# Kernel optimization log

Measured on AMD Instinct MI355X. Metric: run time of the kernel, lower is better.

The kernel has to match this reference:

```python
import jax, jax.numpy as jnp
import numpy as np
import math

B, S, DIM = 1, 2048, 4096
N_HEADS, N_KV, HEAD_DIM = 32, 8, 128
WINDOW = 2048
ROPE_THETA = 10000.0


def setup_inputs() -> dict:
    key = jax.random.key(0)
    ks = jax.random.split(key, 6)
    w_std = 0.02
    x = jax.random.normal(ks[0], (B, S, DIM), dtype=jnp.float32)
    wq = jax.random.normal(ks[1], (DIM, N_HEADS * HEAD_DIM), dtype=jnp.float32) * w_std
    wk = jax.random.normal(ks[2], (DIM, N_KV * HEAD_DIM), dtype=jnp.float32) * w_std
    wv = jax.random.normal(ks[3], (DIM, N_KV * HEAD_DIM), dtype=jnp.float32) * w_std
    wo = jax.random.normal(ks[4], (N_HEADS * HEAD_DIM, DIM), dtype=jnp.float32) * w_std
    # rotary tables (real/imag of complex_rotary_matrix)
    pos = jnp.arange(S, dtype=jnp.float32)
    inv_freq = 1.0 / (ROPE_THETA ** (jnp.arange(0, HEAD_DIM, 2, dtype=jnp.float32) / HEAD_DIM))
    angles = pos[:, None] * inv_freq[None, :]  # [S, HEAD_DIM/2]
    cos, sin = jnp.cos(angles), jnp.sin(angles)
    positions = jnp.arange(S, dtype=jnp.int32)
    # sliding-window causal additive mask: allow j <= i and i - j < WINDOW
    i = jnp.arange(S)[:, None]
    j = jnp.arange(S)[None, :]
    allowed = (j <= i) & (i - j < WINDOW)
    mask = jnp.where(allowed, 0.0, -jnp.inf).astype(jnp.float32)
    cache_k = jnp.zeros((B, WINDOW, N_KV, HEAD_DIM), dtype=jnp.float32)
    cache_v = jnp.zeros((B, WINDOW, N_KV, HEAD_DIM), dtype=jnp.float32)
    return dict(x=x, wq=wq, wk=wk, wv=wv, wo=wo, cos=cos, sin=sin,
                positions=positions, mask=mask, cache_k=cache_k, cache_v=cache_v)


def _apply_rope(t, cos, sin):
    # t: [B, S, H, D]; interleaved complex pairs as in torch.view_as_complex
    tp = t.reshape(*t.shape[:-1], HEAD_DIM // 2, 2)
    te, to = tp[..., 0], tp[..., 1]
    c = cos[None, :, None, :]
    s = sin[None, :, None, :]
    re = te * c - to * s
    im = te * s + to * c
    return jnp.stack([re, im], axis=-1).reshape(t.shape)


def reference(x, wq, wk, wv, wo, cos, sin, positions, mask, cache_k, cache_v):
    repeats = N_HEADS // N_KV
    q = (x @ wq).reshape(B, S, N_HEADS, HEAD_DIM)
    k = (x @ wk).reshape(B, S, N_KV, HEAD_DIM)
    v = (x @ wv).reshape(B, S, N_KV, HEAD_DIM)
    q = _apply_rope(q, cos, sin)
    k = _apply_rope(k, cos, sin)
    # rolling KV-cache scatter update (prefill path: positions.shape[0] > 1)
    scatter_pos = positions[-WINDOW:] % WINDOW
    new_cache_k = cache_k.at[:, scatter_pos].set(k[:, -WINDOW:])
    new_cache_v = cache_v.at[:, scatter_pos].set(v[:, -WINDOW:])
    # GQA head repetition (repeat_kv_head)
    k = jnp.repeat(k, repeats, axis=2)  # [B, S, N_HEADS, D]
    v = jnp.repeat(v, repeats, axis=2)
    scores = jnp.einsum('bqhd,bkhd->bhqk', q, k) / math.sqrt(HEAD_DIM)
    scores = scores + mask[None, None, :, :]
    attn = jax.nn.softmax(scores.astype(jnp.float32), axis=-1).astype(q.dtype)
    out = jnp.einsum('bhqk,bkhd->bqhd', attn, v)
    out = out.reshape(B, S, N_HEADS * HEAD_DIM)
    return out @ wo, new_cache_k, new_cache_v
```

## Files before the change

### kernel.cpp

```cpp
#include <hip/hip_runtime.h>

typedef __bf16 bf16;
typedef __bf16 bf16x8 __attribute__((ext_vector_type(8)));
typedef __bf16 bf16x4 __attribute__((ext_vector_type(4)));
typedef float  f32x4  __attribute__((ext_vector_type(4)));

__device__ __forceinline__ f32x4 mfma16(bf16x8 a, bf16x8 b, f32x4 c) {
  return __builtin_amdgcn_mfma_f32_16x16x32_bf16(a, b, c, 0, 0, 0);
}

__device__ __forceinline__ void gload16(const bf16* g, bf16* l) {
  __builtin_amdgcn_global_load_lds(
      (const __attribute__((address_space(1))) void*)g,
      (__attribute__((address_space(3))) void*)l, 16, 0, 0);
}

__device__ __forceinline__ void tc64_body(const float* __restrict__ in,
                                          bf16* __restrict__ out,
                                          int ldin, int ldout, int bx, int by,
                                          bf16 (*t)[68]) {
  const int c0 = bx * 64, r0 = by * 64;
  const int g4 = threadIdx.x & 15;
  const int q  = threadIdx.x >> 4;
  #pragma unroll
  for (int i = 0; i < 4; ++i) {
    const int r = q + i * 16;
    const float4 v = *(const float4*)&in[(size_t)(r0 + r) * ldin + c0 + g4 * 4];
    bf16x4 b;
    b[0] = (bf16)v.x; b[1] = (bf16)v.y; b[2] = (bf16)v.z; b[3] = (bf16)v.w;
    *(bf16x4*)&t[r][g4 * 4] = b;
  }
  __syncthreads();
  #pragma unroll
  for (int i = 0; i < 4; ++i) {
    const int c = q + i * 16;
    bf16x4 b;
    b[0] = t[g4 * 4 + 0][c]; b[1] = t[g4 * 4 + 1][c];
    b[2] = t[g4 * 4 + 2][c]; b[3] = t[g4 * 4 + 3][c];
    *(bf16x4*)&out[(size_t)(c0 + c) * ldout + r0 + g4 * 4] = b;
  }
}

__global__ void prep1(const float* __restrict__ x, bf16* __restrict__ xb,
                      const float* __restrict__ wq, const float* __restrict__ wk,
                      const float* __restrict__ wv, bf16* __restrict__ wT) {
  __shared__ bf16 t[64][68];
  const int b = blockIdx.x;
  if (b < 8192) {
    const int i = b * 256 + threadIdx.x;
    const float4 v = ((const float4*)x)[i];
    bf16x4 o;
    o[0] = (bf16)v.x; o[1] = (bf16)v.y; o[2] = (bf16)v.z; o[3] = (bf16)v.w;
    *(bf16x4*)&xb[(size_t)i * 4] = o;
  } else if (b < 12288) {
    const int bb = b - 8192;
    tc64_body(wq, wT, 4096, 4096, bb & 63, bb >> 6, t);
  } else if (b < 13312) {
    const int bb = b - 12288;
    tc64_body(wk, wT + (size_t)16777216, 1024, 4096, bb & 15, bb >> 4, t);
  } else {
    const int bb = b - 13312;
    tc64_body(wv, wT + (size_t)20971520, 1024, 4096, bb & 15, bb >> 4, t);
  }
}

__global__ void prep2(bf16* __restrict__ qkv, bf16* __restrict__ kp,
                      float* __restrict__ ck, bf16* __restrict__ vp,
                      float* __restrict__ cv, const float* __restrict__ wo,
                      bf16* __restrict__ wT, const float* __restrict__ cs,
                      const float* __restrict__ sn) {
  __shared__ bf16 t[64][68];
  const int b = blockIdx.x;
  if (b < 16384) {
    const int idx = b * 256 + threadIdx.x;
    const int p  = idx & 63;
    const int sh = idx >> 6;
    const int h  = sh & 31;
    const int s  = sh >> 5;
    const float c  = cs[s * 64 + p];
    const float si = sn[s * 64 + p];
    const size_t ii = (size_t)s * 6144 + h * 128 + 2 * p;
    const float te = (float)qkv[ii], to = (float)qkv[ii + 1];
    qkv[ii]     = (bf16)(te * c - to * si);
    qkv[ii + 1] = (bf16)(te * si + to * c);
  } else if (b < 20480) {
    const int idx = (b - 16384) * 256 + threadIdx.x;
    const int p  = idx & 63;
    const int sh = idx >> 6;
    const int h  = sh & 7;
    const int s  = sh >> 3;
    const float c  = cs[s * 64 + p];
    const float si = sn[s * 64 + p];
    const size_t ii = (size_t)s * 6144 + 4096 + h * 128 + 2 * p;
    const float te = (float)qkv[ii], to = (float)qkv[ii + 1];
    const float re = te * c - to * si;
    const float im = te * si + to * c;
    const size_t io = ((size_t)(h * 4 + (p >> 4)) * 2048 + s) * 32 + ((2 * p) & 31);
    kp[io]     = (bf16)re;
    kp[io + 1] = (bf16)im;
    const size_t ic = (size_t)s * 1024 + h * 128 + 2 * p;
    ck[ic]     = re;
    ck[ic + 1] = im;
  } else if (b < 22528) {
    bf16 (*t32)[33] = (bf16(*)[33])&t[0][0];
    const int bb  = b - 20480;
    const int sb  = bb & 63;
    const int yy  = bb >> 6;
    const int kvh = yy >> 2;
    const int dt  = yy & 3;
    const int x = threadIdx.x & 31, y = threadIdx.x >> 5;
    #pragma unroll
    for (int i = 0; i < 32; i += 8) {
      const bf16 v = qkv[(size_t)(sb * 32 + y + i) * 6144 + 5120 +
                         kvh * 128 + dt * 32 + x];
      t32[y + i][x] = v;
      cv[(size_t)(sb * 32 + y + i) * 1024 + kvh * 128 + dt * 32 + x] = (float)v;
    }
    __syncthreads();
    #pragma unroll
    for (int i = 0; i < 32; i += 8)
      vp[((size_t)(kvh * 64 + sb) * 128 + dt * 32 + y + i) * 32 + x] = t32[x][y + i];
  } else {
    const int bb = b - 22528;
    tc64_body(wo, wT, 4096, 4096, bb & 63, bb >> 6, t);
  }
}

#define MMQ(MB, NB)                                                            \
  _Pragma("unroll")                                                            \
  for (int mi = 0; mi < 4; ++mi)                                               \
    _Pragma("unroll")                                                          \
    for (int ni = 0; ni < 2; ++ni)                                             \
      _Pragma("unroll")                                                        \
      for (int kk = 0; kk < 2; ++kk)                                           \
        acc[MB + mi][NB + ni] =                                                \
            mfma16(ar[mi][kk], br[NB + ni][kk], acc[MB + mi][NB + ni]);

#define MMQ1(MB)                                                               \
  _Pragma("unroll")                                                            \
  for (int mi = 0; mi < 4; ++mi)                                               \
    _Pragma("unroll")                                                          \
    for (int kk = 0; kk < 2; ++kk)                                             \
      acc[MB + mi][2] = mfma16(ar[mi][kk], br[2][kk], acc[MB + mi][2]);

#define PH_OPEN                                                                \
  __builtin_amdgcn_s_barrier();                                                \
  asm volatile("s_waitcnt lgkmcnt(0)" ::: "memory");                           \
  __builtin_amdgcn_s_setprio(1);

#define PH_CLOSE                                                               \
  __builtin_amdgcn_s_setprio(0);                                               \
  __builtin_amdgcn_s_barrier();

template <typename OutT, int NSPLIT>
__global__ __launch_bounds__(512, 2)
void gemm8(const bf16* __restrict__ A, const bf16* __restrict__ Bt,
           OutT* __restrict__ C0, OutT* __restrict__ C1,
           int M, int N, int K, int ldc) {
  __shared__ __attribute__((aligned(16))) bf16 lds[65536];
  char* ldsc = (char*)lds;
  constexpr int AO0 = 0, BO0 = 32768, AO1 = 65536, BO1 = 98304;

  const int t    = threadIdx.x;
  const int w    = t >> 6;
  const int lane = t & 63;
  const int l15  = lane & 15;
  const int lg   = lane >> 4;
  const int wm   = w >> 2;
  const int wn   = w & 3;
  const int hb   = wn >> 1;

  const int nbm = M >> 8;
  const int nb2 = nbm * NSPLIT;
  const int cpx = (nb2 * (N >> 8)) >> 3;
  const int lid = ((int)blockIdx.x & 7) * cpx + ((int)blockIdx.x >> 3);
  const int bn  = (lid / nb2) * 256;
  const int rem = lid % nb2;
  const int kh  = rem / nbm;
  const int bm  = (rem % nbm) * 256;
  const int Kloc = K / NSPLIT;
  const int koff = kh * Kloc;
  OutT* __restrict__ C = (NSPLIT == 2 && kh) ? C1 : C0;

  const int d0     = t * 16;
  const int dsw    = d0 ^ (((d0 >> 9) & 1) << 5);
  const int srow_s = (dsw >> 6) & 127;
  const int scol_e = (dsw & 63) >> 1;

  auto stg = [&](const bf16* P, int rowbase, int tile, int half, int region) {
    const bf16* s = P + (size_t)(rowbase + half * 128 + srow_s) * K +
                    koff + tile * 64 + scol_e;
    gload16(s,      (bf16*)(ldsc + region + half * 16384 + w * 1024));
    gload16(s + 32, (bf16*)(ldsc + region + half * 16384 + 8192 + w * 1024));
  };
  auto lda = [&](int AO, int m, int kk) -> bf16x8 {
    int byte = AO + wm * 16384 + kk * 8192 + (m * 16 + l15) * 64 + lg * 16;
    byte ^= ((byte >> 9) & 1) << 5;
    return *(const bf16x8*)(ldsc + byte);
  };
  auto ldb = [&](int BO, int n, int kk) -> bf16x8 {
    int byte = BO + hb * 16384 + kk * 8192 +
               ((wn & 1) * 64 + n * 16 + l15) * 64 + lg * 16;
    byte ^= ((byte >> 9) & 1) << 5;
    return *(const bf16x8*)(ldsc + byte);
  };

  f32x4 acc[8][4] = {};
  bf16x8 ar[4][2], br[4][2];

  const int NT = Kloc >> 6;
  const int NI = Kloc >> 7;

  stg(A,  bm, 0, 0, AO0);  stg(A,  bm, 0, 1, AO0);
  stg(Bt, bn, 0, 0, BO0);  stg(Bt, bn, 0, 1, BO0);
  stg(Bt, bn, 1, 0, BO1);  stg(Bt, bn, 1, 1, BO1);
  asm volatile("s_waitcnt vmcnt(4)" ::: "memory");
  __builtin_amdgcn_s_barrier();

  #pragma unroll 1
  for (int it = 0; it < NI; ++it) {
    const int t1 = 2 * it + 1;
    const int t2 = (2 * it + 2 < NT) ? 2 * it + 2 : NT - 1;
    const int t3 = (2 * it + 3 < NT) ? 2 * it + 3 : NT - 1;

    #pragma unroll
    for (int mi = 0; mi < 4; ++mi) {
      ar[mi][0] = lda(AO0, mi, 0); ar[mi][1] = lda(AO0, mi, 1);
    }
    #pragma unroll
    for (int ni = 0; ni < 2; ++ni) {
      br[ni][0] = ldb(BO0, ni, 0); br[ni][1] = ldb(BO0, ni, 1);
    }
    stg(A, bm, t1, 0, AO1);
    PH_OPEN; MMQ(0, 0); PH_CLOSE;
    #pragma unroll
    for (int ni = 2; ni < 4; ++ni) {
      br[ni][0] = ldb(BO0, ni, 0); br[ni][1] = ldb(BO0, ni, 1);
    }
    stg(A, bm, t1, 1, AO1);
    PH_OPEN; MMQ(0, 2); PH_CLOSE;
    #pragma unroll
    for (int mi = 0; mi < 4; ++mi) {
      ar[mi][0] = lda(AO0, 4 + mi, 0); ar[mi][1] = lda(AO0, 4 + mi, 1);
    }
    stg(Bt, bn, t2, 0, BO0);
    PH_OPEN; MMQ(4, 0); PH_CLOSE;
    stg(Bt, bn, t2, 1, BO0);
    PH_OPEN; MMQ(4, 2);
    __builtin_amdgcn_s_setprio(0);
    asm volatile("s_waitcnt vmcnt(4)" ::: "memory");
    __builtin_amdgcn_s_barrier();
    #pragma unroll
    for (int mi = 0; mi < 4; ++mi) {
      ar[mi][0] = lda(AO1, mi, 0); ar[mi][1] = lda(AO1, mi, 1);
    }
    #pragma unroll
    for (int ni = 0; ni < 2; ++ni) {
      br[ni][0] = ldb(BO1, ni, 0); br[ni][1] = ldb(BO1, ni, 1);
    }
    stg(A, bm, t2, 0, AO0);
    PH_OPEN; MMQ(0, 0); PH_CLOSE;
    #pragma unroll
    for (int ni = 2; ni < 4; ++ni) {
      br[ni][0] = ldb(BO1, ni, 0); br[ni][1] = ldb(BO1, ni, 1);
    }
    stg(A, bm, t2, 1, AO0);
    PH_OPEN; MMQ(0, 2); PH_CLOSE;
    #pragma unroll
    for (int mi = 0; mi < 4; ++mi) {
      ar[mi][0] = lda(AO1, 4 + mi, 0); ar[mi][1] = lda(AO1, 4 + mi, 1);
    }
    stg(Bt, bn, t3, 0, BO1);
    PH_OPEN; MMQ(4, 0); PH_CLOSE;
    stg(Bt, bn, t3, 1, BO1);
    PH_OPEN; MMQ(4, 2);
    __builtin_amdgcn_s_setprio(0);
    asm volatile("s_waitcnt vmcnt(4)" ::: "memory");
    __builtin_amdgcn_s_barrier();
  }

  #pragma unroll
  for (int mi = 0; mi < 8; ++mi)
    #pragma unroll
    for (int ni = 0; ni < 4; ++ni)
      #pragma unroll
      for (int rr = 0; rr < 4; ++rr)
        C[(size_t)(bm + wm * 128 + mi * 16 + lg * 4 + rr) * ldc +
          (bn + wn * 64 + ni * 16 + l15)] = (OutT)acc[mi][ni][rr];
}

__global__ __launch_bounds__(512, 2)
void gemm8n192(const bf16* __restrict__ A, const bf16* __restrict__ Bt,
               bf16* __restrict__ C, int M, int N, int K, int ldc) {
  __shared__ __attribute__((aligned(16))) bf16 lds[57344];
  char* ldsc = (char*)lds;
  constexpr int AO0 = 0, BO0 = 32768, AO1 = 57344, BO1 = 90112;

  const int t    = threadIdx.x;
  const int w    = t >> 6;
  const int lane = t & 63;
  const int l15  = lane & 15;
  const int lg   = lane >> 4;
  const int wm   = w >> 2;
  const int wn   = w & 3;

  const int cpx = 32;
  const int lid = ((int)blockIdx.x & 7) * cpx + ((int)blockIdx.x >> 3);
  const int bn  = (lid >> 3) * 192;
  const int bm  = (lid & 7) * 256;

  const int d0     = t * 16;
  const int dsw    = d0 ^ (((d0 >> 9) & 1) << 5);
  const int srow_a = (dsw >> 6) & 127;
  const int scol_e = (dsw & 63) >> 1;
  const int rw_b   = (t >> 2) & 63;
  const int kk_b   = t >> 8;

  auto stga = [&](int tile, int half, int region) {
    const bf16* s = A + (size_t)(bm + half * 128 + srow_a) * K + tile * 64 + scol_e;
    gload16(s,      (bf16*)(ldsc + region + half * 16384 + w * 1024));
    gload16(s + 32, (bf16*)(ldsc + region + half * 16384 + 8192 + w * 1024));
  };
  auto stgb = [&](int tile, int third, int region) {
    const bf16* s = Bt + (size_t)(bn + third * 64 + rw_b) * K +
                    tile * 64 + kk_b * 32 + scol_e;
    gload16(s, (bf16*)(ldsc + region + third * 8192 + w * 1024));
  };
  auto lda = [&](int AO, int m, int kk) -> bf16x8 {
    int byte = AO + wm * 16384 + kk * 8192 + (m * 16 + l15) * 64 + lg * 16;
    byte ^= ((byte >> 9) & 1) << 5;
    return *(const bf16x8*)(ldsc + byte);
  };
  auto ldb = [&](int BO, int n, int kk) -> bf16x8 {
    const int row = wn * 48 + n * 16 + l15;
    int byte = BO + (row >> 6) * 8192 + kk * 4096 + (row & 63) * 64 + lg * 16;
    byte ^= ((byte >> 9) & 1) << 5;
    return *(const bf16x8*)(ldsc + byte);
  };

  f32x4 acc[8][3] = {};
  bf16x8 ar[4][2], br[3][2];

  const int NT = K >> 6;
  const int NI = K >> 7;

  stga(0, 0, AO0); stga(0, 1, AO0);
  stgb(0, 0, BO0); stgb(0, 1, BO0); stgb(0, 2, BO0);
  stgb(1, 0, BO1); stgb(1, 1, BO1); stgb(1, 2, BO1);
  asm volatile("s_waitcnt vmcnt(3)" ::: "memory");
  __builtin_amdgcn_s_barrier();

  #pragma unroll 1
  for (int it = 0; it < NI; ++it) {
    const int t1 = 2 * it + 1;
    const int t2 = (2 * it + 2 < NT) ? 2 * it + 2 : NT - 1;
    const int t3 = (2 * it + 3 < NT) ? 2 * it + 3 : NT - 1;

    #pragma unroll
    for (int mi = 0; mi < 4; ++mi) {
      ar[mi][0] = lda(AO0, mi, 0); ar[mi][1] = lda(AO0, mi, 1);
    }
    #pragma unroll
    for (int ni = 0; ni < 2; ++ni) {
      br[ni][0] = ldb(BO0, ni, 0); br[ni][1] = ldb(BO0, ni, 1);
    }
    stga(t1, 0, AO1);
    PH_OPEN; MMQ(0, 0); PH_CLOSE;
    br[2][0] = ldb(BO0, 2, 0); br[2][1] = ldb(BO0, 2, 1);
    stga(t1, 1, AO1);
    PH_OPEN; MMQ1(0); PH_CLOSE;
    #pragma unroll
    for (int mi = 0; mi < 4; ++mi) {
      ar[mi][0] = lda(AO0, 4 + mi, 0); ar[mi][1] = lda(AO0, 4 + mi, 1);
    }
    stgb(t2, 0, BO0); stgb(t2, 1, BO0);
    PH_OPEN; MMQ(4, 0); PH_CLOSE;
    stgb(t2, 2, BO0);
    PH_OPEN; MMQ1(4);
    __builtin_amdgcn_s_setprio(0);
    asm volatile("s_waitcnt vmcnt(3)" ::: "memory");
    __builtin_amdgcn_s_barrier();
    #pragma unroll
    for (int mi = 0; mi < 4; ++mi) {
      ar[mi][0] = lda(AO1, mi, 0); ar[mi][1] = lda(AO1, mi, 1);
    }
    #pragma unroll
    for (int ni = 0; ni < 2; ++ni) {
      br[ni][0] = ldb(BO1, ni, 0); br[ni][1] = ldb(BO1, ni, 1);
    }
    stga(t2, 0, AO0);
    PH_OPEN; MMQ(0, 0); PH_CLOSE;
    br[2][0] = ldb(BO1, 2, 0); br[2][1] = ldb(BO1, 2, 1);
    stga(t2, 1, AO0);
    PH_OPEN; MMQ1(0); PH_CLOSE;
    #pragma unroll
    for (int mi = 0; mi < 4; ++mi) {
      ar[mi][0] = lda(AO1, 4 + mi, 0); ar[mi][1] = lda(AO1, 4 + mi, 1);
    }
    stgb(t3, 0, BO1); stgb(t3, 1, BO1);
    PH_OPEN; MMQ(4, 0); PH_CLOSE;
    stgb(t3, 2, BO1);
    PH_OPEN; MMQ1(4);
    __builtin_amdgcn_s_setprio(0);
    asm volatile("s_waitcnt vmcnt(3)" ::: "memory");
    __builtin_amdgcn_s_barrier();
  }

  #pragma unroll
  for (int mi = 0; mi < 8; ++mi)
    #pragma unroll
    for (int ni = 0; ni < 3; ++ni)
      #pragma unroll
      for (int rr = 0; rr < 4; ++rr)
        C[(size_t)(bm + wm * 128 + mi * 16 + lg * 4 + rr) * ldc +
          (bn + wn * 48 + ni * 16 + l15)] = (bf16)acc[mi][ni][rr];
}

__global__ void reduce_out(const bf16* __restrict__ p0, const bf16* __restrict__ p1,
                           float* __restrict__ out) {
  const int i = blockIdx.x * 256 + threadIdx.x;
  const bf16x4 a = *(const bf16x4*)&p0[(size_t)i * 4];
  const bf16x4 b = *(const bf16x4*)&p1[(size_t)i * 4];
  float4 o;
  o.x = (float)a[0] + (float)b[0];
  o.y = (float)a[1] + (float)b[1];
  o.z = (float)a[2] + (float)b[2];
  o.w = (float)a[3] + (float)b[3];
  *(float4*)&out[(size_t)i * 4] = o;
}

__global__ __launch_bounds__(256, 3)
void attn_fwd(const bf16* __restrict__ Q, const bf16* __restrict__ Kp,
              const bf16* __restrict__ Vp, bf16* __restrict__ O) {
  __shared__ __attribute__((aligned(16))) bf16 Kb[8192];
  __shared__ __attribute__((aligned(16))) bf16 Vb[8192];
  __shared__ __attribute__((aligned(16))) bf16 P_lds[4][16][72];
  const int id   = blockIdx.x;
  const int qt   = 31 - (id >> 5);
  const int kvh  = id & 7;
  const int sub  = (id >> 3) & 3;
  const int h    = kvh * 4 + sub;
  const int t    = threadIdx.x;
  const int w    = t >> 6;
  const int lane = t & 63;
  const int l15  = lane & 15;
  const int lg   = lane >> 4;
  const float scale = 0.08838834764831845f;
  const bf16* Kh = Kp + (size_t)kvh * 262144;
  const bf16* Vh = Vp + (size_t)kvh * 262144;
  const int koff = (t >> 2) * 32 + (t & 3) * 8;

  const int qw  = qt * 64 + w * 16;
  const int myq = qw + l15;

  bf16x8 qf[4];
  #pragma unroll
  for (int ds = 0; ds < 4; ++ds)
    qf[ds] = *(const bf16x8*)&Q[(size_t)myq * 6144 + h * 128 + ds * 32 + lg * 8];

  f32x4 o[8] = {};
  float m = -1e30f, ell = 0.f;

  #pragma unroll
  for (int i = 0; i < 4; ++i)
    gload16(Kh + (size_t)i * 65536 + koff, Kb + i * 2048 + w * 512);
  #pragma unroll
  for (int i = 0; i < 4; ++i)
    gload16(Vh + (size_t)i * 2048 + koff, Vb + i * 2048 + w * 512);
  __syncthreads();

  #pragma unroll 1
  for (int kt = 0; kt <= qt; ++kt) {
    f32x4 T[4] = {};
    __builtin_amdgcn_s_setprio(1);
    #pragma unroll
    for (int kb = 0; kb < 4; ++kb)
      #pragma unroll
      for (int ds = 0; ds < 4; ++ds) {
        bf16x8 kf = *(const bf16x8*)&Kb[(ds * 64 + kb * 16 + l15) * 32 + lg * 8];
        T[kb] = mfma16(kf, qf[ds], T[kb]);
      }
    __builtin_amdgcn_s_setprio(0);
    __syncthreads();
    if (kt < qt) {
      #pragma unroll
      for (int i = 0; i < 4; ++i)
        gload16(Kh + (size_t)i * 65536 + (kt + 1) * 2048 + koff,
                Kb + i * 2048 + w * 512);
    }

    float pv[16];
    float pmax = -1e30f;
    if (kt == qt) {
      #pragma unroll
      for (int kb = 0; kb < 4; ++kb)
        #pragma unroll
        for (int r = 0; r < 4; ++r) {
          const int key = qt * 64 + kb * 16 + lg * 4 + r;
          const float s = (key > myq) ? -1e30f : T[kb][r] * scale;
          pv[kb * 4 + r] = s;
          pmax = fmaxf(pmax, s);
        }
    } else {
      #pragma unroll
      for (int kb = 0; kb < 4; ++kb)
        #pragma unroll
        for (int r = 0; r < 4; ++r) {
          const float s = T[kb][r] * scale;
          pv[kb * 4 + r] = s;
          pmax = fmaxf(pmax, s);
        }
    }
    float base = m;
    if (!__all(pmax - m <= 8.f)) {
      float wmax = pmax;
      wmax = fmaxf(wmax, __shfl_xor(wmax, 16));
      wmax = fmaxf(wmax, __shfl_xor(wmax, 32));
      const float newm = fmaxf(m, wmax);
      const float corr = __expf(m - newm);
      ell *= corr;
      m = newm; base = newm;
      float sf[4];
      #pragma unroll
      for (int r = 0; r < 4; ++r) sf[r] = __shfl(corr, lg * 4 + r);
      #pragma unroll
      for (int df = 0; df < 8; ++df)
        #pragma unroll
        for (int r = 0; r < 4; ++r) o[df][r] *= sf[r];
    }
    bf16 pb[16];
    float tsum = 0.f;
    #pragma unroll
    for (int i = 0; i < 16; ++i) {
      const float p = __expf(pv[i] - base);
      tsum += p;
      pb[i] = (bf16)p;
    }
    ell += tsum;

    #pragma unroll
    for (int kb = 0; kb < 4; ++kb) {
      bf16x4 pk;
      pk[0] = pb[kb * 4 + 0]; pk[1] = pb[kb * 4 + 1];
      pk[2] = pb[kb * 4 + 2]; pk[3] = pb[kb * 4 + 3];
      *(bf16x4*)&P_lds[w][l15][kb * 16 + lg * 4] = pk;
    }
    __builtin_amdgcn_s_setprio(1);
    #pragma unroll
    for (int ks = 0; ks < 2; ++ks) {
      bf16x8 pa = *(const bf16x8*)&P_lds[w][l15][ks * 32 + lg * 8];
      #pragma unroll
      for (int df = 0; df < 8; ++df) {
        bf16x8 vf = *(const bf16x8*)&Vb[(ks * 128 + df * 16 + l15) * 32 + lg * 8];
        o[df] = mfma16(pa, vf, o[df]);
      }
    }
    __builtin_amdgcn_s_setprio(0);
    __syncthreads();
    if (kt < qt) {
      #pragma unroll
      for (int i = 0; i < 4; ++i)
        gload16(Vh + (size_t)(kt + 1) * 8192 + i * 2048 + koff,
                Vb + i * 2048 + w * 512);
    }
  }

  ell += __shfl_xor(ell, 16);
  ell += __shfl_xor(ell, 32);
  float er[4];
  #pragma unroll
  for (int r = 0; r < 4; ++r) er[r] = 1.f / __shfl(ell, lg * 4 + r);
  #pragma unroll
  for (int df = 0; df < 8; ++df)
    #pragma unroll
    for (int r = 0; r < 4; ++r)
      O[(size_t)(qw + lg * 4 + r) * 4096 + h * 128 + df * 16 + l15] =
          (bf16)(o[df][r] * er[r]);
}

extern "C" void kernel_launch(void* const* d_in, const int* in_sizes, int n_in,
                              void* d_out, int out_size, void* d_ws, size_t ws_size,
                              hipStream_t stream) {
  const float* x    = (const float*)d_in[0];
  const float* wq   = (const float*)d_in[1];
  const float* wk   = (const float*)d_in[2];
  const float* wv   = (const float*)d_in[3];
  const float* wo   = (const float*)d_in[4];
  const float* cosf_ = (const float*)d_in[5];
  const float* sinf_ = (const float*)d_in[6];

  float* out     = (float*)d_out;
  float* cache_k = out + (size_t)8388608;
  float* cache_v = cache_k + (size_t)2097152;
  bf16* qkv = (bf16*)d_out;

  bf16* ws = (bf16*)d_ws;
  bf16* wT = ws;
  bf16* kp = ws + (size_t)25165824;
  bf16* vp = kp + (size_t)2097152;
  bf16* xb = vp + (size_t)2097152;
  bf16* aout = xb;
  bf16* part1 = wT + (size_t)16777216;
  bf16* part0 = ws + (size_t)37748736;

  prep1<<<14336, 256, 0, stream>>>(x, xb, wq, wk, wv, wT);
  gemm8n192<<<256, 512, 0, stream>>>(xb, wT, qkv, 2048, 6144, 4096, 6144);
  prep2<<<26624, 256, 0, stream>>>(qkv, kp, cache_k, vp, cache_v, wo, wT,
                                   cosf_, sinf_);
  attn_fwd<<<1024, 256, 0, stream>>>(qkv, kp, vp, aout);
  gemm8<bf16, 2><<<256, 512, 0, stream>>>(aout, wT, part0, part1,
                                          2048, 4096, 4096, 4096);
  reduce_out<<<8192, 256, 0, stream>>>(part0, part1, out);
}
```

Measured before the change: 294.1 us.

## Replace split-K output GEMM and reduce with 256x128-tile GEMM writing fp32

The output projection used to split K across two halves with 256x256 tiles, writing two bf16 partial buffers that a separate kernel summed into fp32. It now uses a new 256x128-tile GEMM over the full K that writes fp32 directly, which still fills 256 blocks. This drops the reduce kernel, the partial-buffer traffic and the bf16 rounding of the partials. The cost is a smaller N-tile, so each block reuses loaded A data less and does twice as many K iterations.

Result: no change. 290.1 us (-1.4%).

```diff
diff --git a/kernel.cpp b/kernel.cpp
--- a/kernel.cpp
+++ b/kernel.cpp
@@ -152,14 +152,12 @@
   __builtin_amdgcn_s_setprio(0);                                               \
   __builtin_amdgcn_s_barrier();
 
-template <typename OutT, int NSPLIT>
 __global__ __launch_bounds__(512, 2)
-void gemm8(const bf16* __restrict__ A, const bf16* __restrict__ Bt,
-           OutT* __restrict__ C0, OutT* __restrict__ C1,
-           int M, int N, int K, int ldc) {
-  __shared__ __attribute__((aligned(16))) bf16 lds[65536];
+void gemm8n192(const bf16* __restrict__ A, const bf16* __restrict__ Bt,
+               bf16* __restrict__ C, int M, int N, int K, int ldc) {
+  __shared__ __attribute__((aligned(16))) bf16 lds[57344];
   char* ldsc = (char*)lds;
-  constexpr int AO0 = 0, BO0 = 32768, AO1 = 65536, BO1 = 98304;
+  constexpr int AO0 = 0, BO0 = 32768, AO1 = 57344, BO1 = 90112;
 
   const int t    = threadIdx.x;
   const int w    = t >> 6;
@@ -168,30 +166,28 @@
   const int lg   = lane >> 4;
   const int wm   = w >> 2;
   const int wn   = w & 3;
-  const int hb   = wn >> 1;
-
-  const int nbm = M >> 8;
-  const int nb2 = nbm * NSPLIT;
-  const int cpx = (nb2 * (N >> 8)) >> 3;
+
+  const int cpx = 32;
   const int lid = ((int)blockIdx.x & 7) * cpx + ((int)blockIdx.x >> 3);
-  const int bn  = (lid / nb2) * 256;
-  const int rem = lid % nb2;
-  const int kh  = rem / nbm;
-  const int bm  = (rem % nbm) * 256;
-  const int Kloc = K / NSPLIT;
-  const int koff = kh * Kloc;
-  OutT* __restrict__ C = (NSPLIT == 2 && kh) ? C1 : C0;
+  const int bn  = (lid >> 3) * 192;
+  const int bm  = (lid & 7) * 256;
 
   const int d0     = t * 16;
   const int dsw    = d0 ^ (((d0 >> 9) & 1) << 5);
-  const int srow_s = (dsw >> 6) & 127;
+  const int srow_a = (dsw >> 6) & 127;
   const int scol_e = (dsw & 63) >> 1;
-
-  auto stg = [&](const bf16* P, int rowbase, int tile, int half, int region) {
-    const bf16* s = P + (size_t)(rowbase + half * 128 + srow_s) * K +
-                    koff + tile * 64 + scol_e;
+  const int rw_b   = (t >> 2) & 63;
+  const int kk_b   = t >> 8;
+
+  auto stga = [&](int tile, int half, int region) {
+    const bf16* s = A + (size_t)(bm + half * 128 + srow_a) * K + tile * 64 + scol_e;
     gload16(s,      (bf16*)(ldsc + region + half * 16384 + w * 1024));
     gload16(s + 32, (bf16*)(ldsc + region + half * 16384 + 8192 + w * 1024));
+  };
+  auto stgb = [&](int tile, int third, int region) {
+    const bf16* s = Bt + (size_t)(bn + third * 64 + rw_b) * K +
+                    tile * 64 + kk_b * 32 + scol_e;
+    gload16(s, (bf16*)(ldsc + region + third * 8192 + w * 1024));
   };
   auto lda = [&](int AO, int m, int kk) -> bf16x8 {
     int byte = AO + wm * 16384 + kk * 8192 + (m * 16 + l15) * 64 + lg * 16;
@@ -199,22 +195,22 @@
     return *(const bf16x8*)(ldsc + byte);
   };
   auto ldb = [&](int BO, int n, int kk) -> bf16x8 {
-    int byte = BO + hb * 16384 + kk * 8192 +
-               ((wn & 1) * 64 + n * 16 + l15) * 64 + lg * 16;
+    const int row = wn * 48 + n * 16 + l15;
+    int byte = BO + (row >> 6) * 8192 + kk * 4096 + (row & 63) * 64 + lg * 16;
     byte ^= ((byte >> 9) & 1) << 5;
     return *(const bf16x8*)(ldsc + byte);
   };
 
-  f32x4 acc[8][4] = {};
-  bf16x8 ar[4][2], br[4][2];
-
-  const int NT = Kloc >> 6;
-  const int NI = Kloc >> 7;
-
-  stg(A,  bm, 0, 0, AO0);  stg(A,  bm, 0, 1, AO0);
-  stg(Bt, bn, 0, 0, BO0);  stg(Bt, bn, 0, 1, BO0);
-  stg(Bt, bn, 1, 0, BO1);  stg(Bt, bn, 1, 1, BO1);
-  asm volatile("s_waitcnt vmcnt(4)" ::: "memory");
+  f32x4 acc[8][3] = {};
+  bf16x8 ar[4][2], br[3][2];
+
+  const int NT = K >> 6;
+  const int NI = K >> 7;
+
+  stga(0, 0, AO0); stga(0, 1, AO0);
+  stgb(0, 0, BO0); stgb(0, 1, BO0); stgb(0, 2, BO0);
+  stgb(1, 0, BO1); stgb(1, 1, BO1); stgb(1, 2, BO1);
+  asm volatile("s_waitcnt vmcnt(3)" ::: "memory");
   __builtin_amdgcn_s_barrier();
 
   #pragma unroll 1
@@ -231,24 +227,21 @@
     for (int ni = 0; ni < 2; ++ni) {
       br[ni][0] = ldb(BO0, ni, 0); br[ni][1] = ldb(BO0, ni, 1);
     }
-    stg(A, bm, t1, 0, AO1);
+    stga(t1, 0, AO1);
     PH_OPEN; MMQ(0, 0); PH_CLOSE;
-    #pragma unroll
-    for (int ni = 2; ni < 4; ++ni) {
-      br[ni][0] = ldb(BO0, ni, 0); br[ni][1] = ldb(BO0, ni, 1);
-    }
-    stg(A, bm, t1, 1, AO1);
-    PH_OPEN; MMQ(0, 2); PH_CLOSE;
+    br[2][0] = ldb(BO0, 2, 0); br[2][1] = ldb(BO0, 2, 1);
+    stga(t1, 1, AO1);
+    PH_OPEN; MMQ1(0); PH_CLOSE;
     #pragma unroll
     for (int mi = 0; mi < 4; ++mi) {
       ar[mi][0] = lda(AO0, 4 + mi, 0); ar[mi][1] = lda(AO0, 4 + mi, 1);
     }
-    stg(Bt, bn, t2, 0, BO0);
+    stgb(t2, 0, BO0); stgb(t2, 1, BO0);
     PH_OPEN; MMQ(4, 0); PH_CLOSE;
-    stg(Bt, bn, t2, 1, BO0);
-    PH_OPEN; MMQ(4, 2);
+    stgb(t2, 2, BO0);
+    PH_OPEN; MMQ1(4);
     __builtin_amdgcn_s_setprio(0);
-    asm volatile("s_waitcnt vmcnt(4)" ::: "memory");
+    asm volatile("s_waitcnt vmcnt(3)" ::: "memory");
     __builtin_amdgcn_s_barrier();
     #pragma unroll
     for (int mi = 0; mi < 4; ++mi) {
@@ -258,43 +251,40 @@
     for (int ni = 0; ni < 2; ++ni) {
       br[ni][0] = ldb(BO1, ni, 0); br[ni][1] = ldb(BO1, ni, 1);
     }
-    stg(A, bm, t2, 0, AO0);
+    stga(t2, 0, AO0);
     PH_OPEN; MMQ(0, 0); PH_CLOSE;
-    #pragma unroll
-    for (int ni = 2; ni < 4; ++ni) {
-      br[ni][0] = ldb(BO1, ni, 0); br[ni][1] = ldb(BO1, ni, 1);
-    }
-    stg(A, bm, t2, 1, AO0);
-    PH_OPEN; MMQ(0, 2); PH_CLOSE;
+    br[2][0] = ldb(BO1, 2, 0); br[2][1] = ldb(BO1, 2, 1);
+    stga(t2, 1, AO0);
+    PH_OPEN; MMQ1(0); PH_CLOSE;
     #pragma unroll
     for (int mi = 0; mi < 4; ++mi) {
       ar[mi][0] = lda(AO1, 4 + mi, 0); ar[mi][1] = lda(AO1, 4 + mi, 1);
     }
-    stg(Bt, bn, t3, 0, BO1);
+    stgb(t3, 0, BO1); stgb(t3, 1, BO1);
     PH_OPEN; MMQ(4, 0); PH_CLOSE;
-    stg(Bt, bn, t3, 1, BO1);
-    PH_OPEN; MMQ(4, 2);
+    stgb(t3, 2, BO1);
+    PH_OPEN; MMQ1(4);
     __builtin_amdgcn_s_setprio(0);
-    asm volatile("s_waitcnt vmcnt(4)" ::: "memory");
+    asm volatile("s_waitcnt vmcnt(3)" ::: "memory");
     __builtin_amdgcn_s_barrier();
   }
 
   #pragma unroll
   for (int mi = 0; mi < 8; ++mi)
     #pragma unroll
-    for (int ni = 0; ni < 4; ++ni)
+    for (int ni = 0; ni < 3; ++ni)
       #pragma unroll
       for (int rr = 0; rr < 4; ++rr)
         C[(size_t)(bm + wm * 128 + mi * 16 + lg * 4 + rr) * ldc +
-          (bn + wn * 64 + ni * 16 + l15)] = (OutT)acc[mi][ni][rr];
+          (bn + wn * 48 + ni * 16 + l15)] = (bf16)acc[mi][ni][rr];
 }
 
 __global__ __launch_bounds__(512, 2)
-void gemm8n192(const bf16* __restrict__ A, const bf16* __restrict__ Bt,
-               bf16* __restrict__ C, int M, int N, int K, int ldc) {
-  __shared__ __attribute__((aligned(16))) bf16 lds[57344];
+void gemm8n128(const bf16* __restrict__ A, const bf16* __restrict__ Bt,
+               float* __restrict__ C, int M, int N, int K, int ldc) {
+  __shared__ __attribute__((aligned(16))) bf16 lds[49152];
   char* ldsc = (char*)lds;
-  constexpr int AO0 = 0, BO0 = 32768, AO1 = 57344, BO1 = 90112;
+  constexpr int AO0 = 0, AO1 = 32768, BO0 = 65536, BO1 = 81920;
 
   const int t    = threadIdx.x;
   const int w    = t >> 6;
@@ -306,25 +296,23 @@
 
   const int cpx = 32;
   const int lid = ((int)blockIdx.x & 7) * cpx + ((int)blockIdx.x >> 3);
-  const int bn  = (lid >> 3) * 192;
+  const int bn  = (lid >> 3) * 128;
   const int bm  = (lid & 7) * 256;
 
   const int d0     = t * 16;
   const int dsw    = d0 ^ (((d0 >> 9) & 1) << 5);
-  const int srow_a = (dsw >> 6) & 127;
+  const int srow_s = (dsw >> 6) & 127;
   const int scol_e = (dsw & 63) >> 1;
-  const int rw_b   = (t >> 2) & 63;
-  const int kk_b   = t >> 8;
 
   auto stga = [&](int tile, int half, int region) {
-    const bf16* s = A + (size_t)(bm + half * 128 + srow_a) * K + tile * 64 + scol_e;
+    const bf16* s = A + (size_t)(bm + half * 128 + srow_s) * K + tile * 64 + scol_e;
     gload16(s,      (bf16*)(ldsc + region + half * 16384 + w * 1024));
     gload16(s + 32, (bf16*)(ldsc + region + half * 16384 + 8192 + w * 1024));
   };
-  auto stgb = [&](int tile, int third, int region) {
-    const bf16* s = Bt + (size_t)(bn + third * 64 + rw_b) * K +
-                    tile * 64 + kk_b * 32 + scol_e;
-    gload16(s, (bf16*)(ldsc + region + third * 8192 + w * 1024));
+  auto stgb = [&](int tile, int region) {
+    const bf16* s = Bt + (size_t)(bn + srow_s) * K + tile * 64 + scol_e;
+    gload16(s,      (bf16*)(ldsc + region + w * 1024));
+    gload16(s + 32, (bf16*)(ldsc + region + 8192 + w * 1024));
   };
   auto lda = [&](int AO, int m, int kk) -> bf16x8 {
     int byte = AO + wm * 16384 + kk * 8192 + (m * 16 + l15) * 64 + lg * 16;
@@ -332,22 +320,22 @@
     return *(const bf16x8*)(ldsc + byte);
   };
   auto ldb = [&](int BO, int n, int kk) -> bf16x8 {
-    const int row = wn * 48 + n * 16 + l15;
-    int byte = BO + (row >> 6) * 8192 + kk * 4096 + (row & 63) * 64 + lg * 16;
+    const int row = wn * 32 + n * 16 + l15;
+    int byte = BO + kk * 8192 + row * 64 + lg * 16;
     byte ^= ((byte >> 9) & 1) << 5;
     return *(const bf16x8*)(ldsc + byte);
   };
 
-  f32x4 acc[8][3] = {};
-  bf16x8 ar[4][2], br[3][2];
+  f32x4 acc[8][2] = {};
+  bf16x8 ar[4][2], br[2][2];
 
   const int NT = K >> 6;
   const int NI = K >> 7;
 
   stga(0, 0, AO0); stga(0, 1, AO0);
-  stgb(0, 0, BO0); stgb(0, 1, BO0); stgb(0, 2, BO0);
-  stgb(1, 0, BO1); stgb(1, 1, BO1); stgb(1, 2, BO1);
-  asm volatile("s_waitcnt vmcnt(3)" ::: "memory");
+  stgb(0, BO0);
+  stgb(1, BO1);
+  asm volatile("s_waitcnt vmcnt(2)" ::: "memory");
   __builtin_amdgcn_s_barrier();
 
   #pragma unroll 1
@@ -366,19 +354,15 @@
     }
     stga(t1, 0, AO1);
     PH_OPEN; MMQ(0, 0); PH_CLOSE;
-    br[2][0] = ldb(BO0, 2, 0); br[2][1] = ldb(BO0, 2, 1);
+    #pragma unroll
+    for (int mi = 0; mi < 4; ++mi) {
+      ar[mi][0] = lda(AO0, 4 + mi, 0); ar[mi][1] = lda(AO0, 4 + mi, 1);
+    }
     stga(t1, 1, AO1);
-    PH_OPEN; MMQ1(0); PH_CLOSE;
-    #pragma unroll
-    for (int mi = 0; mi < 4; ++mi) {
-      ar[mi][0] = lda(AO0, 4 + mi, 0); ar[mi][1] = lda(AO0, 4 + mi, 1);
-    }
-    stgb(t2, 0, BO0); stgb(t2, 1, BO0);
-    PH_OPEN; MMQ(4, 0); PH_CLOSE;
-    stgb(t2, 2, BO0);
-    PH_OPEN; MMQ1(4);
+    stgb(t2, BO0);
+    PH_OPEN; MMQ(4, 0);
     __builtin_amdgcn_s_setprio(0);
-    asm volatile("s_waitcnt vmcnt(3)" ::: "memory");
+    asm volatile("s_waitcnt vmcnt(2)" ::: "memory");
     __builtin_amdgcn_s_barrier();
     #pragma unroll
     for (int mi = 0; mi < 4; ++mi) {
@@ -390,43 +374,26 @@
     }
     stga(t2, 0, AO0);
     PH_OPEN; MMQ(0, 0); PH_CLOSE;
-    br[2][0] = ldb(BO1, 2, 0); br[2][1] = ldb(BO1, 2, 1);
+    #pragma unroll
+    for (int mi = 0; mi < 4; ++mi) {
+      ar[mi][0] = lda(AO1, 4 + mi, 0); ar[mi][1] = lda(AO1, 4 + mi, 1);
+    }
     stga(t2, 1, AO0);
-    PH_OPEN; MMQ1(0); PH_CLOSE;
-    #pragma unroll
-    for (int mi = 0; mi < 4; ++mi) {
-      ar[mi][0] = lda(AO1, 4 + mi, 0); ar[mi][1] = lda(AO1, 4 + mi, 1);
-    }
-    stgb(t3, 0, BO1); stgb(t3, 1, BO1);
-    PH_OPEN; MMQ(4, 0); PH_CLOSE;
-    stgb(t3, 2, BO1);
-    PH_OPEN; MMQ1(4);
+    stgb(t3, BO1);
+    PH_OPEN; MMQ(4, 0);
     __builtin_amdgcn_s_setprio(0);
-    asm volatile("s_waitcnt vmcnt(3)" ::: "memory");
+    asm volatile("s_waitcnt vmcnt(2)" ::: "memory");
     __builtin_amdgcn_s_barrier();
   }
 
   #pragma unroll
   for (int mi = 0; mi < 8; ++mi)
     #pragma unroll
-    for (int ni = 0; ni < 3; ++ni)
+    for (int ni = 0; ni < 2; ++ni)
       #pragma unroll
       for (int rr = 0; rr < 4; ++rr)
         C[(size_t)(bm + wm * 128 + mi * 16 + lg * 4 + rr) * ldc +
-          (bn + wn * 48 + ni * 16 + l15)] = (bf16)acc[mi][ni][rr];
-}
-
-__global__ void reduce_out(const bf16* __restrict__ p0, const bf16* __restrict__ p1,
-                           float* __restrict__ out) {
-  const int i = blockIdx.x * 256 + threadIdx.x;
-  const bf16x4 a = *(const bf16x4*)&p0[(size_t)i * 4];
-  const bf16x4 b = *(const bf16x4*)&p1[(size_t)i * 4];
-  float4 o;
-  o.x = (float)a[0] + (float)b[0];
-  o.y = (float)a[1] + (float)b[1];
-  o.z = (float)a[2] + (float)b[2];
-  o.w = (float)a[3] + (float)b[3];
-  *(float4*)&out[(size_t)i * 4] = o;
+          (bn + wn * 32 + ni * 16 + l15)] = acc[mi][ni][rr];
 }
 
 __global__ __launch_bounds__(256, 3)
@@ -600,15 +567,11 @@
   bf16* vp = kp + (size_t)2097152;
   bf16* xb = vp + (size_t)2097152;
   bf16* aout = xb;
-  bf16* part1 = wT + (size_t)16777216;
-  bf16* part0 = ws + (size_t)37748736;
 
   prep1<<<14336, 256, 0, stream>>>(x, xb, wq, wk, wv, wT);
   gemm8n192<<<256, 512, 0, stream>>>(xb, wT, qkv, 2048, 6144, 4096, 6144);
   prep2<<<26624, 256, 0, stream>>>(qkv, kp, cache_k, vp, cache_v, wo, wT,
                                    cosf_, sinf_);
   attn_fwd<<<1024, 256, 0, stream>>>(qkv, kp, vp, aout);
-  gemm8<bf16, 2><<<256, 512, 0, stream>>>(aout, wT, part0, part1,
-                                          2048, 4096, 4096, 4096);
-  reduce_out<<<8192, 256, 0, stream>>>(part0, part1, out);
-}
+  gemm8n128<<<256, 512, 0, stream>>>(aout, wT, out, 2048, 4096, 4096, 4096);
+}
```
